# Kernel optimization log

Measured on AMD Instinct MI355X. Metric: run time of the kernel, lower is better.

The kernel has to match this reference:

```python
import jax, jax.numpy as jnp
import numpy as np

B, J, D = 1024, 17, 512          # batch, joints, encoder hidden dim
M, K, DT = 34, 2048, 512         # tokens per pose, codebook size, token dim
DDEC, DDEC_I = 32, 64            # decoder hidden dims
L_ENC, L_DEC = 4, 1
DECAY = 0.9
EPS = 1e-5


def _ln(x, g, b):
    m = jnp.mean(x, -1, keepdims=True)
    v = jnp.mean((x - m) ** 2, -1, keepdims=True)
    return (x - m) * jax.lax.rsqrt(v + EPS) * g + b


def _mlp(x, w1, b1, w2, b2):
    return jax.nn.gelu(x @ w1 + b1, approximate=False) @ w2 + b2


def _mixer(x, p, i):
    ln1g, ln1b, tw1, tb1, tw2, tb2, ln2g, ln2b, cw1, cb1, cw2, cb2 = (a[i] for a in p)
    y = jnp.swapaxes(_ln(x, ln1g, ln1b), 1, 2)        # token-mixing over joints
    y = jnp.swapaxes(_mlp(y, tw1, tb1, tw2, tb2), 1, 2)
    z = _mlp(_ln(x + y, ln2g, ln2b), cw1, cb1, cw2, cb2)  # channel-mixing
    return x + y + z


def _forward(joints, invisible_token, start_w, start_b,
             enc_ln1_g, enc_ln1_b, enc_tw1, enc_tb1, enc_tw2, enc_tb2,
             enc_ln2_g, enc_ln2_b, enc_cw1, enc_cb1, enc_cw2, enc_cb2,
             enc_ln_g, enc_ln_b, token_mlp_w, token_mlp_b, feat_w, feat_b,
             dec_ln1_g, dec_ln1_b, dec_tw1, dec_tb1, dec_tw2, dec_tb2,
             dec_ln2_g, dec_ln2_b, dec_cw1, dec_cb1, dec_cw2, dec_cb2,
             dec_token_mlp_w, dec_token_mlp_b, dec_start_w, dec_start_b,
             dec_ln_g, dec_ln_b, rec_w, rec_b,
             codebook, ema_cluster_size, ema_w):
    x = joints[:, :, :2] @ start_w + start_b                  # [B,J,D]
    vis = (joints[:, :, 2:] != 0).astype(x.dtype)             # [B,J,1]
    x = x * vis + invisible_token * (1.0 - vis)
    encp = (enc_ln1_g, enc_ln1_b, enc_tw1, enc_tb1, enc_tw2, enc_tb2,
            enc_ln2_g, enc_ln2_b, enc_cw1, enc_cb1, enc_cw2, enc_cb2)
    for i in range(L_ENC):
        x = _mixer(x, encp, i)
    x = _ln(x, enc_ln_g, enc_ln_b)
    # token_mlp: Linear over joints axis: [B,D,J] -> [B,D,M] -> [B,M,D]
    x = jnp.einsum('bjd,jm->bmd', x, token_mlp_w) + token_mlp_b[None, :, None]
    feat = (x @ feat_w + feat_b).reshape(B * M, DT)           # encode_feat [N,DT]
    # squared euclidean distances to codebook entries
    dists = (jnp.sum(feat * feat, 1, keepdims=True)
             + jnp.sum(codebook * codebook, 1)
             - 2.0 * feat @ codebook.T)                       # [N,K]
    idx = jnp.argmin(dists, axis=1)                           # [N]
    quant = codebook[idx]                                     # == one_hot(idx) @ codebook
    # EMA codebook update (buffers; single-device so all_reduce == identity)
    sg_feat = jax.lax.stop_gradient(feat)
    counts = jax.ops.segment_sum(jnp.ones((B * M,), feat.dtype), idx, num_segments=K)
    dw = jax.ops.segment_sum(sg_feat, idx, num_segments=K)    # == encodings.T @ feat
    cs = ema_cluster_size * DECAY + (1.0 - DECAY) * counts
    n = jnp.sum(cs)
    cs = (cs + 1e-5) / (n + K * 1e-5) * n                     # laplace smoothing
    ema_w_new = ema_w * DECAY + (1.0 - DECAY) * dw
    codebook_new = ema_w_new / cs[:, None]
    e_latent_loss = jnp.mean(jnp.square(jax.lax.stop_gradient(quant) - feat))
    quant = feat + jax.lax.stop_gradient(quant - feat)        # straight-through
    ptf = quant.reshape(B, M, DT)
    out_ptf = jax.lax.stop_gradient(ptf)
    # decoder_token_mlp: Linear over token axis: [B,DT,M] -> [B,DT,J] -> [B,J,DT]
    y = jnp.einsum('bmd,mj->bjd', ptf, dec_token_mlp_w) + dec_token_mlp_b[None, :, None]
    y = y @ dec_start_w + dec_start_b                         # [B,J,DDEC]
    decp = (dec_ln1_g, dec_ln1_b, dec_tw1, dec_tb1, dec_tw2, dec_tb2,
            dec_ln2_g, dec_ln2_b, dec_cw1, dec_cb1, dec_cw2, dec_cb2)
    for i in range(L_DEC):
        y = _mixer(y, decp, i)
    y = _ln(y, dec_ln_g, dec_ln_b)
    rec = y @ rec_w + rec_b                                   # [B,J,2]
    return rec, idx, e_latent_loss, out_ptf, codebook_new


def setup_inputs():
    ks = iter(jax.random.split(jax.random.key(0), 64))
    def nrm(shape, s=0.02):
        return jax.random.normal(next(ks), shape, jnp.float32) * s
    inp = {}
    coords = jax.random.uniform(next(ks), (B, J, 2), jnp.float32)
    inp['joints'] = jnp.concatenate([coords, jnp.ones((B, J, 1), jnp.float32)], -1)
    inp['joints_feature'] = nrm((B, J, 256), 1.0)   # unused (guide_ratio=0)
    inp['cls_logits'] = jnp.zeros((1, 1), jnp.float32)  # unused in tokenizer stage
    inp['invisible_token'] = nrm((1, 1, D))
    inp['start_w'], inp['start_b'] = nrm((2, D)), jnp.zeros((D,), jnp.float32)
    for pre, L, H, HI in (('enc', L_ENC, D, D), ('dec', L_DEC, DDEC, DDEC_I)):
        inp[pre + '_ln1_g'], inp[pre + '_ln1_b'] = jnp.ones((L, H)), jnp.zeros((L, H))
        inp[pre + '_tw1'], inp[pre + '_tb1'] = nrm((L, J, 64)), jnp.zeros((L, 64))
        inp[pre + '_tw2'], inp[pre + '_tb2'] = nrm((L, 64, J)), jnp.zeros((L, J))
        inp[pre + '_ln2_g'], inp[pre + '_ln2_b'] = jnp.ones((L, H)), jnp.zeros((L, H))
        inp[pre + '_cw1'], inp[pre + '_cb1'] = nrm((L, H, HI)), jnp.zeros((L, HI))
        inp[pre + '_cw2'], inp[pre + '_cb2'] = nrm((L, HI, H)), jnp.zeros((L, H))
    inp['enc_ln_g'], inp['enc_ln_b'] = jnp.ones((D,)), jnp.zeros((D,))
    inp['token_mlp_w'], inp['token_mlp_b'] = nrm((J, M)), jnp.zeros((M,))
    inp['feat_w'], inp['feat_b'] = nrm((D, DT)), jnp.zeros((DT,))
    inp['codebook'] = jax.random.normal(next(ks), (K, DT), jnp.float32)
    inp['ema_cluster_size'] = jnp.zeros((K,), jnp.float32)
    inp['ema_w'] = jax.random.normal(next(ks), (K, DT), jnp.float32)
    inp['dec_token_mlp_w'], inp['dec_token_mlp_b'] = nrm((M, J)), jnp.zeros((J,))
    inp['dec_start_w'], inp['dec_start_b'] = nrm((DT, DDEC)), jnp.zeros((DDEC,))
    inp['dec_ln_g'], inp['dec_ln_b'] = jnp.ones((DDEC,)), jnp.zeros((DDEC,))
    inp['rec_w'], inp['rec_b'] = nrm((DDEC, 2)), jnp.zeros((2,))
    return inp


def reference(joints, joints_feature, cls_logits, invisible_token, start_w, start_b,
              enc_ln1_g, enc_ln1_b, enc_tw1, enc_tb1, enc_tw2, enc_tb2,
              enc_ln2_g, enc_ln2_b, enc_cw1, enc_cb1, enc_cw2, enc_cb2,
              enc_ln_g, enc_ln_b, token_mlp_w, token_mlp_b, feat_w, feat_b,
              codebook, ema_cluster_size, ema_w,
              dec_ln1_g, dec_ln1_b, dec_tw1, dec_tb1, dec_tw2, dec_tb2,
              dec_ln2_g, dec_ln2_b, dec_cw1, dec_cb1, dec_cw2, dec_cb2,
              dec_token_mlp_w, dec_token_mlp_b, dec_start_w, dec_start_b,
              dec_ln_g, dec_ln_b, rec_w, rec_b):
    # joints_feature / cls_logits unused: guide_ratio=0, stage_pct='tokenizer'
    return _forward(joints, invisible_token, start_w, start_b,
                    enc_ln1_g, enc_ln1_b, enc_tw1, enc_tb1, enc_tw2, enc_tb2,
                    enc_ln2_g, enc_ln2_b, enc_cw1, enc_cb1, enc_cw2, enc_cb2,
                    enc_ln_g, enc_ln_b, token_mlp_w, token_mlp_b, feat_w, feat_b,
                    dec_ln1_g, dec_ln1_b, dec_tw1, dec_tb1, dec_tw2, dec_tb2,
                    dec_ln2_g, dec_ln2_b, dec_cw1, dec_cb1, dec_cw2, dec_cb2,
                    dec_token_mlp_w, dec_token_mlp_b, dec_start_w, dec_start_b,
                    dec_ln_g, dec_ln_b, rec_w, rec_b,
                    codebook, ema_cluster_size, ema_w)
```

## Files before the change

### kernel.cpp

```cpp
#include <hip/hip_runtime.h>
#include <math.h>

constexpr int Bn = 1024, Jn = 17, Mn = 34;
constexpr int RJ = Bn * Jn;
constexpr int RM = Bn * Mn;
constexpr size_t SZX = (size_t)RJ * 512;
constexpr size_t SZM = (size_t)RM * 512;

typedef __attribute__((ext_vector_type(8))) short bf16x8;
typedef __attribute__((ext_vector_type(4))) float f32x4;
typedef unsigned long long u64;
typedef unsigned short u16;
typedef unsigned int u32;

__device__ __forceinline__ float gelu_f(float x) {
  return 0.5f * x * (1.0f + erff(x * 0.7071067811865475f));
}
__device__ __forceinline__ u16 bf16_rne(float x) {
  u32 u = __float_as_uint(x);
  u += 0x7fffu + ((u >> 16) & 1u);
  return (u16)(u >> 16);
}
__device__ __forceinline__ float bf16_f(u16 h) {
  return __uint_as_float((u32)h << 16);
}

typedef __attribute__((address_space(1))) const void gas_t;
typedef __attribute__((address_space(3))) void las_t;
__device__ __forceinline__ void gll16(const void* g, void* l) {
  __builtin_amdgcn_global_load_lds((gas_t*)g, (las_t*)l, 16, 0, 0);
}

__global__ __launch_bounds__(256) void embed_kernel(
    const float* __restrict__ joints, const float* __restrict__ inv,
    const float* __restrict__ sw, const float* __restrict__ sb,
    float* __restrict__ out) {
  int tid = blockIdx.x * 256 + threadIdx.x;
  int row = tid >> 9, d = tid & 511;
  float j0 = joints[row * 3 + 0];
  float j1 = joints[row * 3 + 1];
  float j2 = joints[row * 3 + 2];
  float x = fmaf(j0, sw[d], fmaf(j1, sw[512 + d], sb[d]));
  float v = (j2 != 0.0f) ? 1.0f : 0.0f;
  out[tid] = x * v + inv[d] * (1.0f - v);
}

__global__ __launch_bounds__(256) void mixer_fused(
    const float* __restrict__ x_in, float* __restrict__ res_out,
    u16* __restrict__ oh, u16* __restrict__ ol,
    const float* __restrict__ g1, const float* __restrict__ b1,
    const float* __restrict__ tw1, const float* __restrict__ tb1,
    const float* __restrict__ tw2, const float* __restrict__ tb2,
    const float* __restrict__ g2, const float* __restrict__ b2,
    const float* __restrict__ W1, const float* __restrict__ W2,
    u16* __restrict__ Th1, u16* __restrict__ Tl1,
    u16* __restrict__ Th2, u16* __restrict__ Tl2) {
  __shared__ float xs[17][512];
  __shared__ float stats[17][2];
  const int tid = threadIdx.x;
  const int b = blockIdx.x;
  {
    int gid = b * 256 + tid;
    int k = gid >> 9, n = gid & 511;
    float v = W1[gid];
    u16 h = bf16_rne(v);
    Th1[(size_t)n * 512 + k] = h;
    Tl1[(size_t)n * 512 + k] = bf16_rne(v - bf16_f(h));
    v = W2[gid];
    h = bf16_rne(v);
    Th2[(size_t)n * 512 + k] = h;
    Tl2[(size_t)n * 512 + k] = bf16_rne(v - bf16_f(h));
  }
  const float* px = x_in + (size_t)b * 17 * 512;
  for (int i = tid; i < 17 * 512; i += 256) xs[i >> 9][i & 511] = px[i];
  __syncthreads();
  const int wv = tid >> 6, ln_ = tid & 63;
  for (int j = wv; j < 17; j += 4) {
    float v[8];
    float s = 0.0f;
#pragma unroll
    for (int i = 0; i < 8; i++) { v[i] = xs[j][ln_ + 64 * i]; s += v[i]; }
#pragma unroll
    for (int m = 32; m; m >>= 1) s += __shfl_xor(s, m);
    float mean = s * (1.0f / 512.0f);
    float s2 = 0.0f;
#pragma unroll
    for (int i = 0; i < 8; i++) { float t = v[i] - mean; s2 += t * t; }
#pragma unroll
    for (int m = 32; m; m >>= 1) s2 += __shfl_xor(s2, m);
    float rs = 1.0f / sqrtf(s2 * (1.0f / 512.0f) + 1e-5f);
    if (ln_ == 0) { stats[j][0] = mean; stats[j][1] = rs; }
  }
  __syncthreads();
  {
    const int d0 = tid, d1 = tid + 256;
    float ga = g1[d0], ba = b1[d0];
    float gb = g1[d1], bb2 = b1[d1];
    float t0[17], t1[17], a0[17], a1[17];
#pragma unroll
    for (int j = 0; j < 17; j++) {
      float mj = stats[j][0], rj = stats[j][1];
      t0[j] = (xs[j][d0] - mj) * rj * ga + ba;
      t1[j] = (xs[j][d1] - mj) * rj * gb + bb2;
      a0[j] = 0.0f; a1[j] = 0.0f;
    }
#pragma unroll 1
    for (int k = 0; k < 64; k++) {
      float h0 = tb1[k], h1 = h0;
#pragma unroll
      for (int j = 0; j < 17; j++) {
        float w = tw1[j * 64 + k];
        h0 = fmaf(t0[j], w, h0);
        h1 = fmaf(t1[j], w, h1);
      }
      h0 = gelu_f(h0);
      h1 = gelu_f(h1);
#pragma unroll
      for (int j = 0; j < 17; j++) {
        float w = tw2[k * 17 + j];
        a0[j] = fmaf(h0, w, a0[j]);
        a1[j] = fmaf(h1, w, a1[j]);
      }
    }
#pragma unroll
    for (int j = 0; j < 17; j++) {
      float tb = tb2[j];
      float r0 = xs[j][d0] + a0[j] + tb;
      float r1 = xs[j][d1] + a1[j] + tb;
      xs[j][d0] = r0;
      xs[j][d1] = r1;
      res_out[((size_t)b * 17 + j) * 512 + d0] = r0;
      res_out[((size_t)b * 17 + j) * 512 + d1] = r1;
    }
  }
  __syncthreads();
  for (int j = wv; j < 17; j += 4) {
    float v[8];
    float s = 0.0f;
#pragma unroll
    for (int i = 0; i < 8; i++) { v[i] = xs[j][ln_ + 64 * i]; s += v[i]; }
#pragma unroll
    for (int m = 32; m; m >>= 1) s += __shfl_xor(s, m);
    float mean = s * (1.0f / 512.0f);
    float s2 = 0.0f;
#pragma unroll
    for (int i = 0; i < 8; i++) { float t = v[i] - mean; s2 += t * t; }
#pragma unroll
    for (int m = 32; m; m >>= 1) s2 += __shfl_xor(s2, m);
    float rs = 1.0f / sqrtf(s2 * (1.0f / 512.0f) + 1e-5f);
#pragma unroll
    for (int i = 0; i < 8; i++) {
      int d = ln_ + 64 * i;
      float o = (v[i] - mean) * rs * g2[d] + b2[d];
      u16 h = bf16_rne(o);
      size_t off = ((size_t)b * 17 + j) * 512 + d;
      oh[off] = h;
      ol[off] = bf16_rne(o - bf16_f(h));
    }
  }
}

__global__ __launch_bounds__(256) void lnmix_fused(
    const float* __restrict__ x_in, u16* __restrict__ oh, u16* __restrict__ ol,
    const float* __restrict__ g, const float* __restrict__ bb,
    const float* __restrict__ w, const float* __restrict__ bias,
    const float* __restrict__ Wf, u16* __restrict__ Thf, u16* __restrict__ Tlf) {
  __shared__ float xs[17][513];
  const int tid = threadIdx.x;
  const int b = blockIdx.x;
  {
    int gid = b * 256 + tid;
    int k = gid >> 9, n = gid & 511;
    float v = Wf[gid];
    u16 h = bf16_rne(v);
    Thf[(size_t)n * 512 + k] = h;
    Tlf[(size_t)n * 512 + k] = bf16_rne(v - bf16_f(h));
  }
  const float* px = x_in + (size_t)b * 17 * 512;
  for (int i = tid; i < 17 * 512; i += 256) xs[i >> 9][i & 511] = px[i];
  __syncthreads();
  const int wv = tid >> 6, ln_ = tid & 63;
  for (int j = wv; j < 17; j += 4) {
    float v[8];
    float s = 0.0f;
#pragma unroll
    for (int i = 0; i < 8; i++) { v[i] = xs[j][ln_ + 64 * i]; s += v[i]; }
#pragma unroll
    for (int m = 32; m; m >>= 1) s += __shfl_xor(s, m);
    float mean = s * (1.0f / 512.0f);
    float s2 = 0.0f;
#pragma unroll
    for (int i = 0; i < 8; i++) { float t = v[i] - mean; s2 += t * t; }
#pragma unroll
    for (int m = 32; m; m >>= 1) s2 += __shfl_xor(s2, m);
    float rs = 1.0f / sqrtf(s2 * (1.0f / 512.0f) + 1e-5f);
#pragma unroll
    for (int i = 0; i < 8; i++) {
      int d = ln_ + 64 * i;
      xs[j][d] = (v[i] - mean) * rs * g[d] + bb[d];
    }
  }
  __syncthreads();
  {
    const int d0 = tid, d1 = tid + 256;
    float t0[17], t1[17];
#pragma unroll
    for (int j = 0; j < 17; j++) { t0[j] = xs[j][d0]; t1[j] = xs[j][d1]; }
#pragma unroll 1
    for (int m = 0; m < 34; m++) {
      float s0 = bias[m], s1 = s0;
#pragma unroll
      for (int j = 0; j < 17; j++) {
        float wv2 = w[j * 34 + m];
        s0 = fmaf(t0[j], wv2, s0);
        s1 = fmaf(t1[j], wv2, s1);
      }
      size_t o0 = ((size_t)b * 34 + m) * 512 + d0;
      u16 h0 = bf16_rne(s0);
      oh[o0] = h0;
      ol[o0] = bf16_rne(s0 - bf16_f(h0));
      size_t o1 = o0 + 256;
      u16 h1 = bf16_rne(s1);
      oh[o1] = h1;
      ol[o1] = bf16_rne(s1 - bf16_f(h1));
    }
  }
}

__global__ __launch_bounds__(256) void splitnorm_kernel(
    const float* __restrict__ CBm, u16* __restrict__ hi, u16* __restrict__ lo,
    float* __restrict__ cnorm, u64* __restrict__ packed, int* __restrict__ cnt) {
  int gid = blockIdx.x * 256 + threadIdx.x;
  for (int i = gid; i < RM; i += 131072) packed[i] = ~0ull;
  if (gid < 2048) cnt[gid] = 0;
  int wave = threadIdx.x >> 6, lane = threadIdx.x & 63;
  int k = blockIdx.x * 4 + wave;
  const float4* p4 = (const float4*)(CBm + (size_t)k * 512);
  ushort4* h4 = (ushort4*)(hi + (size_t)k * 512);
  ushort4* l4 = (ushort4*)(lo + (size_t)k * 512);
  float s = 0.0f;
#pragma unroll
  for (int i = 0; i < 2; i++) {
    float4 x = p4[lane + 64 * i];
    ushort4 h, l;
    h.x = bf16_rne(x.x); l.x = bf16_rne(x.x - bf16_f(h.x));
    h.y = bf16_rne(x.y); l.y = bf16_rne(x.y - bf16_f(h.y));
    h.z = bf16_rne(x.z); l.z = bf16_rne(x.z - bf16_f(h.z));
    h.w = bf16_rne(x.w); l.w = bf16_rne(x.w - bf16_f(h.w));
    h4[lane + 64 * i] = h;
    l4[lane + 64 * i] = l;
    s = fmaf(x.x, x.x, s); s = fmaf(x.y, x.y, s);
    s = fmaf(x.z, x.z, s); s = fmaf(x.w, x.w, s);
  }
#pragma unroll
  for (int m = 32; m; m >>= 1) s += __shfl_xor(s, m);
  if (lane == 0) cnorm[k] = s;
}

template <int GELU_FLAG, int RES_FLAG, int HILO_OUT>
__global__ __launch_bounds__(256, 4) void mgemm64(
    const u16* __restrict__ Ah, const u16* __restrict__ Al,
    const u16* __restrict__ Bh, const u16* __restrict__ Bl,
    const float* __restrict__ bias, const float* __restrict__ R,
    float* __restrict__ C, u16* __restrict__ Oh, u16* __restrict__ Ol, int N) {
  __shared__ __align__(16) u16 sAh[2048], sAl[2048], sBh[4096], sBl[4096];
  const int tid = threadIdx.x;
  const int m0 = blockIdx.x * 64, n0 = blockIdx.y * 128;
  const int lane = tid & 63, wave = tid >> 6;
  const int wm = wave >> 1, wn = wave & 1;
  const int fr = lane & 15, q = lane >> 4;
  const int ra = tid >> 2, ca = (tid & 3) ^ ((ra >> 1) & 3);
  const size_t aoff = (size_t)(m0 + ra) * 512 + ca * 8;
  const int rb0 = tid >> 2, cb0 = (tid & 3) ^ ((rb0 >> 1) & 3);
  const int ci1 = tid + 256;
  const int rb1 = ci1 >> 2, cb1 = (ci1 & 3) ^ ((rb1 >> 1) & 3);
  const size_t boff0 = (size_t)(n0 + rb0) * 512 + cb0 * 8;
  const size_t boff1 = (size_t)(n0 + rb1) * 512 + cb1 * 8;
  const int ldA = wave * 512;
  const int ldB0 = wave * 512, ldB1 = 2048 + wave * 512;
  int fca[2], fcb[4];
#pragma unroll
  for (int mt = 0; mt < 2; mt++) {
    int rra = wm * 32 + mt * 16 + fr;
    fca[mt] = (rra * 4 + (q ^ ((rra >> 1) & 3))) * 8;
  }
#pragma unroll
  for (int nt = 0; nt < 4; nt++) {
    int rrb = wn * 64 + nt * 16 + fr;
    fcb[nt] = (rrb * 4 + (q ^ ((rrb >> 1) & 3))) * 8;
  }
  f32x4 acc[2][4];
#pragma unroll
  for (int i = 0; i < 2; i++)
#pragma unroll
    for (int j = 0; j < 4; j++) {
      acc[i][j][0] = 0.0f; acc[i][j][1] = 0.0f;
      acc[i][j][2] = 0.0f; acc[i][j][3] = 0.0f;
    }
  for (int k0 = 0; k0 < 512; k0 += 32) {
    gll16(Ah + aoff + k0, &sAh[ldA]);
    gll16(Al + aoff + k0, &sAl[ldA]);
    gll16(Bh + boff0 + k0, &sBh[ldB0]);
    gll16(Bh + boff1 + k0, &sBh[ldB1]);
    gll16(Bl + boff0 + k0, &sBl[ldB0]);
    gll16(Bl + boff1 + k0, &sBl[ldB1]);
    __syncthreads();
    bf16x8 fah[2], fal[2], fbh[4], fbl[4];
#pragma unroll
    for (int mt = 0; mt < 2; mt++) {
      fah[mt] = *(const bf16x8*)&sAh[fca[mt]];
      fal[mt] = *(const bf16x8*)&sAl[fca[mt]];
    }
#pragma unroll
    for (int nt = 0; nt < 4; nt++) {
      fbh[nt] = *(const bf16x8*)&sBh[fcb[nt]];
      fbl[nt] = *(const bf16x8*)&sBl[fcb[nt]];
    }
#pragma unroll
    for (int mt = 0; mt < 2; mt++)
#pragma unroll
      for (int nt = 0; nt < 4; nt++) {
        acc[mt][nt] = __builtin_amdgcn_mfma_f32_16x16x32_bf16(
            fah[mt], fbh[nt], acc[mt][nt], 0, 0, 0);
        acc[mt][nt] = __builtin_amdgcn_mfma_f32_16x16x32_bf16(
            fah[mt], fbl[nt], acc[mt][nt], 0, 0, 0);
        acc[mt][nt] = __builtin_amdgcn_mfma_f32_16x16x32_bf16(
            fal[mt], fbh[nt], acc[mt][nt], 0, 0, 0);
      }
    __syncthreads();
  }
#pragma unroll
  for (int mt = 0; mt < 2; mt++)
#pragma unroll
    for (int reg = 0; reg < 4; reg++) {
      int row = m0 + wm * 32 + mt * 16 + q * 4 + reg;
#pragma unroll
      for (int nt = 0; nt < 4; nt++) {
        int col = n0 + wn * 64 + nt * 16 + fr;
        float v = acc[mt][nt][reg] + bias[col];
        if (GELU_FLAG) v = gelu_f(v);
        if (RES_FLAG) v += R[(size_t)row * N + col];
        if (HILO_OUT) {
          u16 h = bf16_rne(v);
          Oh[(size_t)row * N + col] = h;
          Ol[(size_t)row * N + col] = bf16_rne(v - bf16_f(h));
        } else {
          C[(size_t)row * N + col] = v;
        }
      }
    }
}

#define MG_PROLOGUE()                                                        \
  const int tid = threadIdx.x;                                               \
  const int m0 = blockIdx.x * 128, n0 = blockIdx.y * 128;                    \
  const int lane = tid & 63, wave = tid >> 6;                                \
  const int wm = wave >> 1, wn = wave & 1;                                   \
  const int fr = lane & 15, q = lane >> 4, qd = q;                           \
  const int ci0 = wave * 128 + lane, ci1 = ci0 + 64;                         \
  const int r0 = ci0 >> 2, c0x = (ci0 & 3) ^ ((r0 >> 1) & 3);                \
  const int r1 = ci1 >> 2, c1x = (ci1 & 3) ^ ((r1 >> 1) & 3);                \
  const size_t aoff0 = (size_t)(m0 + r0) * 512 + c0x * 8;                    \
  const size_t aoff1 = (size_t)(m0 + r1) * 512 + c1x * 8;                    \
  const size_t boff0 = (size_t)(n0 + r0) * 512 + c0x * 8;                    \
  const size_t boff1 = (size_t)(n0 + r1) * 512 + c1x * 8;                    \
  const int ld0 = wave * 1024, ld1 = ld0 + 512;       \
  int fca[4], fcb[4];                                                        \
  _Pragma("unroll") for (int t4 = 0; t4 < 4; t4++) {                         \
    int rra = wm * 64 + t4 * 16 + fr;                                        \
    int rrb = wn * 64 + t4 * 16 + fr;                                        \
    int sz = q ^ ((fr >> 1) & 3);                                            \
    fca[t4] = (rra * 4 + sz) * 8;                                            \
    fcb[t4] = (rrb * 4 + sz) * 8;                                            \
  }                                                                          \
  f32x4 acc[4][4];                                                           \
  _Pragma("unroll") for (int i = 0; i < 4; i++)                              \
    _Pragma("unroll") for (int j = 0; j < 4; j++) {                          \
      acc[i][j][0] = 0.0f; acc[i][j][1] = 0.0f;                              \
      acc[i][j][2] = 0.0f; acc[i][j][3] = 0.0f;                              \
    }

#define MG_KLOOP(Ah, Al, Bh, Bl)                                             \
  for (int k0 = 0; k0 < 512; k0 += 32) {                                     \
    gll16(Ah + aoff0 + k0, &sAh[ld0]);                                       \
    gll16(Ah + aoff1 + k0, &sAh[ld1]);                                       \
    gll16(Al + aoff0 + k0, &sAl[ld0]);                                       \
    gll16(Al + aoff1 + k0, &sAl[ld1]);                                       \
    gll16(Bh + boff0 + k0, &sBh[ld0]);                                       \
    gll16(Bh + boff1 + k0, &sBh[ld1]);                                       \
    gll16(Bl + boff0 + k0, &sBl[ld0]);                                       \
    gll16(Bl + boff1 + k0, &sBl[ld1]);                                       \
    __syncthreads();                                                         \
    bf16x8 fah[4], fal[4], fbh[4], fbl[4];                                   \
    _Pragma("unroll") for (int t4 = 0; t4 < 4; t4++) {                       \
      fah[t4] = *(const bf16x8*)&sAh[fca[t4]];                               \
      fal[t4] = *(const bf16x8*)&sAl[fca[t4]];                               \
      fbh[t4] = *(const bf16x8*)&sBh[fcb[t4]];                               \
      fbl[t4] = *(const bf16x8*)&sBl[fcb[t4]];                               \
    }                                                                        \
    _Pragma("unroll") for (int mt = 0; mt < 4; mt++)                         \
      _Pragma("unroll") for (int nt = 0; nt < 4; nt++) {                     \
        acc[mt][nt] = __builtin_amdgcn_mfma_f32_16x16x32_bf16(               \
            fah[mt], fbh[nt], acc[mt][nt], 0, 0, 0);                         \
        acc[mt][nt] = __builtin_amdgcn_mfma_f32_16x16x32_bf16(               \
            fah[mt], fbl[nt], acc[mt][nt], 0, 0, 0);                         \
        acc[mt][nt] = __builtin_amdgcn_mfma_f32_16x16x32_bf16(               \
            fal[mt], fbh[nt], acc[mt][nt], 0, 0, 0);                         \
      }                                                                      \
    __syncthreads();                                                         \
  }

__global__ __launch_bounds__(256, 4) void dist_mfma(
    const u16* __restrict__ Ah, const u16* __restrict__ Al,
    const u16* __restrict__ Bh, const u16* __restrict__ Bl,
    const float* __restrict__ cnorm, u64* __restrict__ packed) {
  __shared__ __align__(16) u16 sAh[4096], sAl[4096], sBh[4096], sBl[4096];
  MG_PROLOGUE()
  MG_KLOOP(Ah, Al, Bh, Bl)
#pragma unroll
  for (int mt = 0; mt < 4; mt++)
#pragma unroll
    for (int reg = 0; reg < 4; reg++) {
      u64 best = ~0ull;
#pragma unroll
      for (int nt = 0; nt < 4; nt++) {
        int c = n0 + wn * 64 + nt * 16 + fr;
        float d = cnorm[c] - 2.0f * acc[mt][nt][reg];
        u32 ub = __float_as_uint(d);
        ub = (ub & 0x80000000u) ? ~ub : (ub | 0x80000000u);
        u64 p = ((u64)ub << 32) | (u32)c;
        best = (p < best) ? p : best;
      }
#pragma unroll
      for (int mm = 1; mm <= 8; mm <<= 1) {
        u32 h2 = __shfl_xor((u32)(best >> 32), mm);
        u32 l2 = __shfl_xor((u32)best, mm);
        u64 o = ((u64)h2 << 32) | l2;
        best = (o < best) ? o : best;
      }
      if (fr == 0) {
        int row = m0 + wm * 64 + mt * 16 + qd * 4 + reg;
        atomicMin(&packed[row], best);
      }
    }
}

__global__ __launch_bounds__(256) void idxcount_kernel(
    const u64* __restrict__ packed, float* __restrict__ o_idx,
    int* __restrict__ cnt) {
  __shared__ int h[2048];
  for (int i = threadIdx.x; i < 2048; i += 256) h[i] = 0;
  __syncthreads();
  int r = blockIdx.x * 256 + threadIdx.x;
  u32 k = (u32)packed[r];
  o_idx[r] = (float)k;
  atomicAdd(&h[k], 1);
  __syncthreads();
  for (int i = threadIdx.x; i < 2048; i += 256) {
    int v = h[i];
    if (v) atomicAdd(&cnt[i], v);
  }
}

__global__ __launch_bounds__(256) void scan_kernel(
    const int* __restrict__ cnt, int* __restrict__ base,
    int* __restrict__ cursor, const float* __restrict__ ema_cs,
    float* __restrict__ nbuf) {
  __shared__ int part[256];
  __shared__ float esum[256];
  int t = threadIdx.x;
  int local[8];
  int s = 0;
  float es = 0.0f;
#pragma unroll
  for (int i = 0; i < 8; i++) {
    local[i] = cnt[t * 8 + i];
    s += local[i];
    es += ema_cs[t * 8 + i];
  }
  part[t] = s;
  esum[t] = es;
  __syncthreads();
  for (int off = 1; off < 256; off <<= 1) {
    int v = (t >= off) ? part[t - off] : 0;
    __syncthreads();
    part[t] += v;
    __syncthreads();
  }
  int run = part[t] - s;
#pragma unroll
  for (int i = 0; i < 8; i++) {
    base[t * 8 + i] = run;
    cursor[t * 8 + i] = run;
    run += local[i];
  }
  for (int o = 128; o; o >>= 1) {
    if (t < o) esum[t] += esum[t + o];
    __syncthreads();
  }
  if (t == 0) nbuf[0] = 0.9f * esum[0] + 0.1f * (float)RM;
}

__global__ __launch_bounds__(256) void scatter_kernel(
    const u64* __restrict__ packed, int* __restrict__ cursor,
    u32* __restrict__ bucket, float* __restrict__ dw) {
  __shared__ int h[2048];
  __shared__ int gb[2048];
  int gid = blockIdx.x * 256 + threadIdx.x;
  for (int i = gid; i < 2048 * 512; i += RM) dw[i] = 0.0f;
  for (int i = threadIdx.x; i < 2048; i += 256) h[i] = 0;
  __syncthreads();
  int k = (int)(u32)packed[gid];
  int lrank = atomicAdd(&h[k], 1);
  __syncthreads();
  for (int i = threadIdx.x; i < 2048; i += 256) {
    int v = h[i];
    gb[i] = v ? atomicAdd(&cursor[i], v) : 0;
  }
  __syncthreads();
  bucket[gb[k] + lrank] = ((u32)k << 17) | (u32)gid;
}

__global__ __launch_bounds__(256) void quant_out_kernel(
    const u16* __restrict__ fh, const u16* __restrict__ fl,
    const float* __restrict__ CBm, const u64* __restrict__ packed,
    float* __restrict__ ptf_out, float* __restrict__ lpart) {
  __shared__ float wred[4];
  int row = blockIdx.x * 2 + (threadIdx.x >> 7);
  int t = threadIdx.x & 127;
  int k = (int)(u32)packed[row];
  uint2 hb = ((const uint2*)(fh + (size_t)row * 512))[t];
  uint2 lb = ((const uint2*)(fl + (size_t)row * 512))[t];
  float f0 = bf16_f((u16)hb.x) + bf16_f((u16)lb.x);
  float f1 = bf16_f((u16)(hb.x >> 16)) + bf16_f((u16)(lb.x >> 16));
  float f2 = bf16_f((u16)hb.y) + bf16_f((u16)lb.y);
  float f3 = bf16_f((u16)(hb.y >> 16)) + bf16_f((u16)(lb.y >> 16));
  float4 c = ((const float4*)(CBm + (size_t)k * 512))[t];
  float* po = ptf_out + (size_t)row * 512 + 4 * t;
  po[0] = c.x; po[1] = c.y; po[2] = c.z; po[3] = c.w;
  float dx = c.x - f0, dy = c.y - f1, dz = c.z - f2, dwv = c.w - f3;
  float ls = dx * dx + dy * dy + dz * dz + dwv * dwv;
#pragma unroll
  for (int m = 32; m; m >>= 1) ls += __shfl_xor(ls, m);
  if ((threadIdx.x & 63) == 0) wred[threadIdx.x >> 6] = ls;
  __syncthreads();
  if (threadIdx.x == 0)
    lpart[blockIdx.x] = wred[0] + wred[1] + wred[2] + wred[3];
}

__global__ __launch_bounds__(256) void dwsum_chunk_kernel(
    const u16* __restrict__ fh, const u16* __restrict__ fl,
    const u32* __restrict__ bucket, float* __restrict__ dw) {
  __shared__ u32 sp[64];
  const int t = threadIdx.x;
  if (t < 64) sp[t] = bucket[blockIdx.x * 64 + t];
  __syncthreads();
  float ax = 0.0f, ay = 0.0f;
  int curk = (int)(sp[0] >> 17);
  u32 hb = *(const u32*)(fh + (size_t)(sp[0] & 0x1FFFF) * 512 + 2 * t);
  u32 lb = *(const u32*)(fl + (size_t)(sp[0] & 0x1FFFF) * 512 + 2 * t);
  for (int i = 0; i < 64; i++) {
    u32 hn = 0, ln2 = 0;
    if (i + 1 < 64) {
      hn = *(const u32*)(fh + (size_t)(sp[i + 1] & 0x1FFFF) * 512 + 2 * t);
      ln2 = *(const u32*)(fl + (size_t)(sp[i + 1] & 0x1FFFF) * 512 + 2 * t);
    }
    int k = (int)(sp[i] >> 17);
    if (k != curk) {
      atomicAdd(&dw[(size_t)curk * 512 + 2 * t], ax);
      atomicAdd(&dw[(size_t)curk * 512 + 2 * t + 1], ay);
      ax = 0.0f; ay = 0.0f; curk = k;
    }
    ax += bf16_f((u16)hb) + bf16_f((u16)lb);
    ay += bf16_f((u16)(hb >> 16)) + bf16_f((u16)(lb >> 16));
    hb = hn; lb = ln2;
  }
  atomicAdd(&dw[(size_t)curk * 512 + 2 * t], ax);
  atomicAdd(&dw[(size_t)curk * 512 + 2 * t + 1], ay);
}

__global__ __launch_bounds__(256) void cbnew_kernel(
    const float* __restrict__ ema_w, const float* __restrict__ dw,
    const float* __restrict__ ema_cs, const int* __restrict__ cnt,
    const float* __restrict__ nbuf, float* __restrict__ outp,
    const float* __restrict__ lpart, float* __restrict__ loss_out) {
  int tid = blockIdx.x * 256 + threadIdx.x;
  int k = tid >> 9;
  float n = nbuf[0];
  float cs = ema_cs[k] * 0.9f + 0.1f * (float)cnt[k];
  cs = (cs + 1e-5f) / (n + 0.02048f) * n;
  outp[tid] = (ema_w[tid] * 0.9f + 0.1f * dw[tid]) / cs;
  if (blockIdx.x == 0) {
    __shared__ float red[256];
    float s = 0.0f;
    for (int i = threadIdx.x; i < RM / 2; i += 256) s += lpart[i];
    red[threadIdx.x] = s;
    __syncthreads();
    for (int o = 128; o; o >>= 1) {
      if (threadIdx.x < o) red[threadIdx.x] += red[threadIdx.x + o];
      __syncthreads();
    }
    if (threadIdx.x == 0)
      loss_out[0] = red[0] / (float)((size_t)RM * 512);
  }
}

__global__ __launch_bounds__(256) void decoder_fused(
    const float* __restrict__ ptf,
    const float* __restrict__ dtokw, const float* __restrict__ dtokb,
    const float* __restrict__ dsw, const float* __restrict__ dsb,
    const float* __restrict__ ln1g, const float* __restrict__ ln1b,
    const float* __restrict__ tw1, const float* __restrict__ tb1,
    const float* __restrict__ tw2, const float* __restrict__ tb2,
    const float* __restrict__ ln2g, const float* __restrict__ ln2b,
    const float* __restrict__ cw1, const float* __restrict__ cb1,
    const float* __restrict__ cw2, const float* __restrict__ cb2,
    const float* __restrict__ lng, const float* __restrict__ lnb,
    const float* __restrict__ recw, const float* __restrict__ recb,
    float* __restrict__ o_rec) {
  __shared__ float yS[17][260];
  __shared__ float zS[17][33];
  __shared__ float t2S[17][33];
  __shared__ float hS[17][65];
  const int tid = threadIdx.x;
  const int b = blockIdx.x;
  float zacc0 = 0.0f, zacc1 = 0.0f, zacc2 = 0.0f;
  const int j0 = tid >> 5, dd0 = tid & 31;
  const int j1 = (tid + 256) >> 5;
  const int j2 = (tid + 512) >> 5;
  for (int ch = 0; ch < 2; ch++) {
    float p[34];
#pragma unroll
    for (int m = 0; m < 34; m++)
      p[m] = ptf[((size_t)b * 34 + m) * 512 + ch * 256 + tid];
#pragma unroll 1
    for (int j = 0; j < 17; j++) {
      float s = dtokb[j];
#pragma unroll
      for (int m = 0; m < 34; m++) s = fmaf(p[m], dtokw[m * 17 + j], s);
      yS[j][tid] = s;
    }
    __syncthreads();
    {
      const float4* y0 = (const float4*)&yS[j0][0];
      const float4* y1 = (const float4*)&yS[j1][0];
      const float* wg = dsw + (size_t)ch * 256 * 32 + dd0;
#pragma unroll 1
      for (int d4 = 0; d4 < 64; d4++) {
        float4 va = y0[d4];
        float4 vb = y1[d4];
        float w0 = wg[(4 * d4 + 0) * 32];
        float w1 = wg[(4 * d4 + 1) * 32];
        float w2 = wg[(4 * d4 + 2) * 32];
        float w3 = wg[(4 * d4 + 3) * 32];
        zacc0 = fmaf(va.x, w0, zacc0); zacc0 = fmaf(va.y, w1, zacc0);
        zacc0 = fmaf(va.z, w2, zacc0); zacc0 = fmaf(va.w, w3, zacc0);
        zacc1 = fmaf(vb.x, w0, zacc1); zacc1 = fmaf(vb.y, w1, zacc1);
        zacc1 = fmaf(vb.z, w2, zacc1); zacc1 = fmaf(vb.w, w3, zacc1);
      }
      if (tid < 32) {
        const float4* y2 = (const float4*)&yS[j2][0];
#pragma unroll 1
        for (int d4 = 0; d4 < 64; d4++) {
          float4 vc = y2[d4];
          float w0 = wg[(4 * d4 + 0) * 32];
          float w1 = wg[(4 * d4 + 1) * 32];
          float w2 = wg[(4 * d4 + 2) * 32];
          float w3 = wg[(4 * d4 + 3) * 32];
          zacc2 = fmaf(vc.x, w0, zacc2); zacc2 = fmaf(vc.y, w1, zacc2);
          zacc2 = fmaf(vc.z, w2, zacc2); zacc2 = fmaf(vc.w, w3, zacc2);
        }
      }
    }
    __syncthreads();
  }
  zS[j0][dd0] = zacc0 + dsb[dd0];
  zS[j1][dd0] = zacc1 + dsb[dd0];
  if (tid < 32) zS[j2][dd0] = zacc2 + dsb[dd0];
  __syncthreads();
  if (tid < 17) {
    float m = 0.0f;
#pragma unroll
    for (int d = 0; d < 32; d++) m += zS[tid][d];
    m *= (1.0f / 32.0f);
    float v = 0.0f;
#pragma unroll
    for (int d = 0; d < 32; d++) { float t = zS[tid][d] - m; v += t * t; }
    float rs = 1.0f / sqrtf(v * (1.0f / 32.0f) + 1e-5f);
#pragma unroll
    for (int d = 0; d < 32; d++)
      t2S[tid][d] = (zS[tid][d] - m) * rs * ln1g[d] + ln1b[d];
  }
  __syncthreads();
  if (tid < 32) {
    float t[17], acc[17];
#pragma unroll
    for (int j = 0; j < 17; j++) { t[j] = t2S[j][tid]; acc[j] = 0.0f; }
    for (int k = 0; k < 64; k++) {
      float h = tb1[k];
#pragma unroll
      for (int j = 0; j < 17; j++) h = fmaf(t[j], tw1[j * 64 + k], h);
      h = gelu_f(h);
#pragma unroll
      for (int j = 0; j < 17; j++) acc[j] = fmaf(h, tw2[k * 17 + j], acc[j]);
    }
#pragma unroll
    for (int j = 0; j < 17; j++) zS[j][tid] = zS[j][tid] + acc[j] + tb2[j];
  }
  __syncthreads();
  if (tid < 17) {
    float m = 0.0f;
#pragma unroll
    for (int d = 0; d < 32; d++) m += zS[tid][d];
    m *= (1.0f / 32.0f);
    float v = 0.0f;
#pragma unroll
    for (int d = 0; d < 32; d++) { float t = zS[tid][d] - m; v += t * t; }
    float rs = 1.0f / sqrtf(v * (1.0f / 32.0f) + 1e-5f);
#pragma unroll
    for (int d = 0; d < 32; d++)
      t2S[tid][d] = (zS[tid][d] - m) * rs * ln2g[d] + ln2b[d];
  }
  __syncthreads();
  for (int p = tid; p < 17 * 64; p += 256) {
    int j = p >> 6, k = p & 63;
    float s = cb1[k];
#pragma unroll
    for (int d = 0; d < 32; d++) s = fmaf(t2S[j][d], cw1[d * 64 + k], s);
    hS[j][k] = gelu_f(s);
  }
  __syncthreads();
  {
    float cb = cb2[dd0];
    float s0 = cb, s1 = cb;
#pragma unroll
    for (int k = 0; k < 64; k++) {
      float w = cw2[k * 32 + dd0];
      s0 = fmaf(hS[j0][k], w, s0);
      s1 = fmaf(hS[j1][k], w, s1);
    }
    zS[j0][dd0] += s0;
    zS[j1][dd0] += s1;
    if (tid < 32) {
      float s2 = cb;
#pragma unroll
      for (int k = 0; k < 64; k++) s2 = fmaf(hS[j2][k], cw2[k * 32 + dd0], s2);
      zS[j2][dd0] += s2;
    }
  }
  __syncthreads();
  if (tid < 17) {
    float m = 0.0f;
#pragma unroll
    for (int d = 0; d < 32; d++) m += zS[tid][d];
    m *= (1.0f / 32.0f);
    float v = 0.0f;
#pragma unroll
    for (int d = 0; d < 32; d++) { float t = zS[tid][d] - m; v += t * t; }
    float rs = 1.0f / sqrtf(v * (1.0f / 32.0f) + 1e-5f);
#pragma unroll
    for (int d = 0; d < 32; d++)
      t2S[tid][d] = (zS[tid][d] - m) * rs * lng[d] + lnb[d];
  }
  __syncthreads();
  if (tid < 34) {
    int j = tid >> 1, c = tid & 1;
    float s = recb[c];
#pragma unroll
    for (int d = 0; d < 32; d++) s = fmaf(t2S[j][d], recw[d * 2 + c], s);
    o_rec[((size_t)b * 17 + j) * 2 + c] = s;
  }
}

extern "C" void kernel_launch(void* const* d_in, const int* in_sizes, int n_in,
                              void* d_out, int out_size, void* d_ws, size_t ws_size,
                              hipStream_t stream) {
  const float* joints   = (const float*)d_in[0];
  const float* inv_tok  = (const float*)d_in[3];
  const float* start_w  = (const float*)d_in[4];
  const float* start_b  = (const float*)d_in[5];
  const float* e_ln1g = (const float*)d_in[6];
  const float* e_ln1b = (const float*)d_in[7];
  const float* e_tw1  = (const float*)d_in[8];
  const float* e_tb1  = (const float*)d_in[9];
  const float* e_tw2  = (const float*)d_in[10];
  const float* e_tb2  = (const float*)d_in[11];
  const float* e_ln2g = (const float*)d_in[12];
  const float* e_ln2b = (const float*)d_in[13];
  const float* e_cw1  = (const float*)d_in[14];
  const float* e_cb1  = (const float*)d_in[15];
  const float* e_cw2  = (const float*)d_in[16];
  const float* e_cb2  = (const float*)d_in[17];
  const float* d_ln1g = (const float*)d_in[18];
  const float* d_ln1b = (const float*)d_in[19];
  const float* d_tw1  = (const float*)d_in[20];
  const float* d_tb1  = (const float*)d_in[21];
  const float* d_tw2  = (const float*)d_in[22];
  const float* d_tb2  = (const float*)d_in[23];
  const float* d_ln2g = (const float*)d_in[24];
  const float* d_ln2b = (const float*)d_in[25];
  const float* d_cw1  = (const float*)d_in[26];
  const float* d_cb1  = (const float*)d_in[27];
  const float* d_cw2  = (const float*)d_in[28];
  const float* d_cb2  = (const float*)d_in[29];
  const float* enc_lng = (const float*)d_in[30];
  const float* enc_lnb = (const float*)d_in[31];
  const float* tok_w   = (const float*)d_in[32];
  const float* tok_b   = (const float*)d_in[33];
  const float* feat_w  = (const float*)d_in[34];
  const float* feat_b  = (const float*)d_in[35];
  const float* codebook = (const float*)d_in[36];
  const float* ema_cs   = (const float*)d_in[37];
  const float* ema_w    = (const float*)d_in[38];
  const float* dtok_w   = (const float*)d_in[39];
  const float* dtok_b   = (const float*)d_in[40];
  const float* dstart_w = (const float*)d_in[41];
  const float* dstart_b = (const float*)d_in[42];
  const float* dec_lng  = (const float*)d_in[43];
  const float* dec_lnb  = (const float*)d_in[44];
  const float* rec_w    = (const float*)d_in[45];
  const float* rec_b    = (const float*)d_in[46];

  float* ws = (float*)d_ws;
  float* Ab  = ws;
  float* Bb  = ws + SZX;
  float* Cc  = ws + 2 * SZX;
  float* P1e = ws + 3 * SZX;
  float* P2e = ws + 4 * SZX;
  float* cbs = ws + 5 * SZX;
  float* cnorm = cbs + 1048576;
  u64*  packed = (u64*)(cnorm + 2048);
  int*  cnt    = (int*)(cnorm + 2048 + 69632);
  int*  basebuf = cnt + 2048;
  int*  cursor  = basebuf + 2048;
  u32*  bucket  = (u32*)(cursor + 2048);
  float* lpart  = (float*)(bucket + RM);
  float* nbuf   = lpart + RM / 2;
  float* dw     = nbuf + 2048;
  u16* WTh1 = (u16*)dw;
  u16* WTl1 = (u16*)(dw + 131072);
  u16* WTh2 = (u16*)(dw + 262144);
  u16* WTl2 = (u16*)(dw + 393216);
  u16* P1eh = (u16*)P1e;  u16* P1el = (u16*)(P1e + SZX / 2);
  u16* P2eh = (u16*)P2e;  u16* P2el = (u16*)(P2e + SZX / 2);
  u16* P1mh = (u16*)Ab;   u16* P1ml = (u16*)Bb;
  u16* P2mh = (u16*)Cc;   u16* P2ml = (u16*)P1e;
  u16* chh = (u16*)cbs;   u16* cll = (u16*)(cbs + 524288);

  float* outp = (float*)d_out;
  float* o_rec = outp;
  float* o_idx = outp + (size_t)RJ * 2;
  float* o_loss = o_idx + RM;
  float* o_ptf = o_loss + 1;
  float* o_cb = o_ptf + SZM;

  embed_kernel<<<(RJ * 512) / 256, 256, 0, stream>>>(joints, inv_tok, start_w, start_b, Ab);
  for (int i = 0; i < 4; i++) {
    mixer_fused<<<Bn, 256, 0, stream>>>(
        Ab, Bb, P1eh, P1el,
        e_ln1g + i * 512, e_ln1b + i * 512,
        e_tw1 + i * 17 * 64, e_tb1 + i * 64, e_tw2 + i * 64 * 17, e_tb2 + i * 17,
        e_ln2g + i * 512, e_ln2b + i * 512,
        e_cw1 + (size_t)i * 512 * 512, e_cw2 + (size_t)i * 512 * 512,
        WTh1, WTl1, WTh2, WTl2);
    mgemm64<1, 0, 1><<<dim3(RJ / 64, 4), 256, 0, stream>>>(
        P1eh, P1el, WTh1, WTl1, e_cb1 + i * 512, nullptr, nullptr, P2eh, P2el, 512);
    mgemm64<0, 1, 0><<<dim3(RJ / 64, 4), 256, 0, stream>>>(
        P2eh, P2el, WTh2, WTl2, e_cb2 + i * 512, Bb, Ab, nullptr, nullptr, 512);
  }
  lnmix_fused<<<Bn, 256, 0, stream>>>(Ab, P1mh, P1ml, enc_lng, enc_lnb, tok_w, tok_b,
                                      feat_w, WTh1, WTl1);
  mgemm64<0, 0, 1><<<dim3(RM / 64, 4), 256, 0, stream>>>(
      P1mh, P1ml, WTh1, WTl1, feat_b, nullptr, nullptr, P2mh, P2ml, 512);

  splitnorm_kernel<<<2048 / 4, 256, 0, stream>>>(codebook, chh, cll, cnorm, packed, cnt);
  dist_mfma<<<dim3(RM / 128, 2048 / 128), 256, 0, stream>>>(P2mh, P2ml, chh, cll, cnorm, packed);

  idxcount_kernel<<<RM / 256, 256, 0, stream>>>(packed, o_idx, cnt);
  scan_kernel<<<1, 256, 0, stream>>>(cnt, basebuf, cursor, ema_cs, nbuf);
  scatter_kernel<<<RM / 256, 256, 0, stream>>>(packed, cursor, bucket, dw);
  quant_out_kernel<<<RM / 2, 256, 0, stream>>>(P2mh, P2ml, codebook, packed, o_ptf, lpart);
  dwsum_chunk_kernel<<<RM / 64, 256, 0, stream>>>(P2mh, P2ml, bucket, dw);
  cbnew_kernel<<<(2048 * 512) / 256, 256, 0, stream>>>(
      ema_w, dw, ema_cs, cnt, nbuf, o_cb, lpart, o_loss);

  decoder_fused<<<Bn, 256, 0, stream>>>(
      o_ptf, dtok_w, dtok_b, dstart_w, dstart_b,
      d_ln1g, d_ln1b, d_tw1, d_tb1, d_tw2, d_tb2, d_ln2g, d_ln2b,
      d_cw1, d_cb1, d_cw2, d_cb2, dec_lng, dec_lnb, rec_w, rec_b, o_rec);
}
```

Baseline: 1.361 ms.

## Fuse embed into first mixer, merge quant output into dwsum, split dist launch

The embedding is now computed directly into shared memory inside the first mixer launch, which removes a separate kernel and a round trip of the activation tensor through global memory. Quantized-output writing and the commitment-loss partial sums move into the bucketed dwsum kernel, so the quant_out kernel and its second read of the features disappear. The codebook-distance kernel is split into two launches over codebook halves, with the occupancy hint raised from 4 to 5 blocks. The split launch relies on atomic-min style packing into the same buffer across both launches, and the loss reduction bound changes to match the new number of partials.

```diff
diff --git a/kernel.cpp b/kernel.cpp
--- a/kernel.cpp
+++ b/kernel.cpp
@@ -31,20 +31,7 @@
   __builtin_amdgcn_global_load_lds((gas_t*)g, (las_t*)l, 16, 0, 0);
 }
 
-__global__ __launch_bounds__(256) void embed_kernel(
-    const float* __restrict__ joints, const float* __restrict__ inv,
-    const float* __restrict__ sw, const float* __restrict__ sb,
-    float* __restrict__ out) {
-  int tid = blockIdx.x * 256 + threadIdx.x;
-  int row = tid >> 9, d = tid & 511;
-  float j0 = joints[row * 3 + 0];
-  float j1 = joints[row * 3 + 1];
-  float j2 = joints[row * 3 + 2];
-  float x = fmaf(j0, sw[d], fmaf(j1, sw[512 + d], sb[d]));
-  float v = (j2 != 0.0f) ? 1.0f : 0.0f;
-  out[tid] = x * v + inv[d] * (1.0f - v);
-}
-
+template <int EMBED>
 __global__ __launch_bounds__(256) void mixer_fused(
     const float* __restrict__ x_in, float* __restrict__ res_out,
     u16* __restrict__ oh, u16* __restrict__ ol,
@@ -54,7 +41,9 @@
     const float* __restrict__ g2, const float* __restrict__ b2,
     const float* __restrict__ W1, const float* __restrict__ W2,
     u16* __restrict__ Th1, u16* __restrict__ Tl1,
-    u16* __restrict__ Th2, u16* __restrict__ Tl2) {
+    u16* __restrict__ Th2, u16* __restrict__ Tl2,
+    const float* __restrict__ joints, const float* __restrict__ inv_tok,
+    const float* __restrict__ swg, const float* __restrict__ sbg) {
   __shared__ float xs[17][512];
   __shared__ float stats[17][2];
   const int tid = threadIdx.x;
@@ -71,8 +60,18 @@
     Th2[(size_t)n * 512 + k] = h;
     Tl2[(size_t)n * 512 + k] = bf16_rne(v - bf16_f(h));
   }
-  const float* px = x_in + (size_t)b * 17 * 512;
-  for (int i = tid; i < 17 * 512; i += 256) xs[i >> 9][i & 511] = px[i];
+  if (EMBED) {
+    for (int i = tid; i < 17 * 512; i += 256) {
+      int j = i >> 9, d = i & 511;
+      const float* jp = joints + ((size_t)b * 17 + j) * 3;
+      float x = fmaf(jp[0], swg[d], fmaf(jp[1], swg[512 + d], sbg[d]));
+      float vis = (jp[2] != 0.0f) ? 1.0f : 0.0f;
+      xs[j][d] = x * vis + inv_tok[d] * (1.0f - vis);
+    }
+  } else {
+    const float* px = x_in + (size_t)b * 17 * 512;
+    for (int i = tid; i < 17 * 512; i += 256) xs[i >> 9][i & 511] = px[i];
+  }
   __syncthreads();
   const int wv = tid >> 6, ln_ = tid & 63;
   for (int j = wv; j < 17; j += 4) {
@@ -353,7 +352,7 @@
 
 #define MG_PROLOGUE()                                                        \
   const int tid = threadIdx.x;                                               \
-  const int m0 = blockIdx.x * 128, n0 = blockIdx.y * 128;                    \
+  const int m0 = blockIdx.x * 128, n0 = (blockIdx.y + n_base) * 128;         \
   const int lane = tid & 63, wave = tid >> 6;                                \
   const int wm = wave >> 1, wn = wave & 1;                                   \
   const int fr = lane & 15, q = lane >> 4, qd = q;                           \
@@ -410,10 +409,10 @@
     __syncthreads();                                                         \
   }
 
-__global__ __launch_bounds__(256, 4) void dist_mfma(
+__global__ __launch_bounds__(256, 5) void dist_mfma(
     const u16* __restrict__ Ah, const u16* __restrict__ Al,
     const u16* __restrict__ Bh, const u16* __restrict__ Bl,
-    const float* __restrict__ cnorm, u64* __restrict__ packed) {
+    const float* __restrict__ cnorm, u64* __restrict__ packed, int n_base) {
   __shared__ __align__(16) u16 sAh[4096], sAl[4096], sBh[4096], sBl[4096];
   MG_PROLOGUE()
   MG_KLOOP(Ah, Al, Bh, Bl)
@@ -521,42 +520,20 @@
   bucket[gb[k] + lrank] = ((u32)k << 17) | (u32)gid;
 }
 
-__global__ __launch_bounds__(256) void quant_out_kernel(
-    const u16* __restrict__ fh, const u16* __restrict__ fl,
-    const float* __restrict__ CBm, const u64* __restrict__ packed,
-    float* __restrict__ ptf_out, float* __restrict__ lpart) {
-  __shared__ float wred[4];
-  int row = blockIdx.x * 2 + (threadIdx.x >> 7);
-  int t = threadIdx.x & 127;
-  int k = (int)(u32)packed[row];
-  uint2 hb = ((const uint2*)(fh + (size_t)row * 512))[t];
-  uint2 lb = ((const uint2*)(fl + (size_t)row * 512))[t];
-  float f0 = bf16_f((u16)hb.x) + bf16_f((u16)lb.x);
-  float f1 = bf16_f((u16)(hb.x >> 16)) + bf16_f((u16)(lb.x >> 16));
-  float f2 = bf16_f((u16)hb.y) + bf16_f((u16)lb.y);
-  float f3 = bf16_f((u16)(hb.y >> 16)) + bf16_f((u16)(lb.y >> 16));
-  float4 c = ((const float4*)(CBm + (size_t)k * 512))[t];
-  float* po = ptf_out + (size_t)row * 512 + 4 * t;
-  po[0] = c.x; po[1] = c.y; po[2] = c.z; po[3] = c.w;
-  float dx = c.x - f0, dy = c.y - f1, dz = c.z - f2, dwv = c.w - f3;
-  float ls = dx * dx + dy * dy + dz * dz + dwv * dwv;
-#pragma unroll
-  for (int m = 32; m; m >>= 1) ls += __shfl_xor(ls, m);
-  if ((threadIdx.x & 63) == 0) wred[threadIdx.x >> 6] = ls;
-  __syncthreads();
-  if (threadIdx.x == 0)
-    lpart[blockIdx.x] = wred[0] + wred[1] + wred[2] + wred[3];
-}
-
 __global__ __launch_bounds__(256) void dwsum_chunk_kernel(
     const u16* __restrict__ fh, const u16* __restrict__ fl,
-    const u32* __restrict__ bucket, float* __restrict__ dw) {
+    const u32* __restrict__ bucket, const float* __restrict__ CBm,
+    float* __restrict__ dw, float* __restrict__ ptf_out,
+    float* __restrict__ lpart) {
   __shared__ u32 sp[64];
+  __shared__ float wred[4];
   const int t = threadIdx.x;
   if (t < 64) sp[t] = bucket[blockIdx.x * 64 + t];
   __syncthreads();
-  float ax = 0.0f, ay = 0.0f;
+  float ax = 0.0f, ay = 0.0f, lacc = 0.0f;
   int curk = (int)(sp[0] >> 17);
+  float c0 = CBm[(size_t)curk * 512 + 2 * t];
+  float c1 = CBm[(size_t)curk * 512 + 2 * t + 1];
   u32 hb = *(const u32*)(fh + (size_t)(sp[0] & 0x1FFFF) * 512 + 2 * t);
   u32 lb = *(const u32*)(fl + (size_t)(sp[0] & 0x1FFFF) * 512 + 2 * t);
   for (int i = 0; i < 64; i++) {
@@ -570,13 +547,27 @@
       atomicAdd(&dw[(size_t)curk * 512 + 2 * t], ax);
       atomicAdd(&dw[(size_t)curk * 512 + 2 * t + 1], ay);
       ax = 0.0f; ay = 0.0f; curk = k;
-    }
-    ax += bf16_f((u16)hb) + bf16_f((u16)lb);
-    ay += bf16_f((u16)(hb >> 16)) + bf16_f((u16)(lb >> 16));
+      c0 = CBm[(size_t)k * 512 + 2 * t];
+      c1 = CBm[(size_t)k * 512 + 2 * t + 1];
+    }
+    float f0 = bf16_f((u16)hb) + bf16_f((u16)lb);
+    float f1 = bf16_f((u16)(hb >> 16)) + bf16_f((u16)(lb >> 16));
+    ax += f0;
+    ay += f1;
+    int row = (int)(sp[i] & 0x1FFFF);
+    ptf_out[(size_t)row * 512 + 2 * t] = c0;
+    ptf_out[(size_t)row * 512 + 2 * t + 1] = c1;
+    float e0 = c0 - f0, e1 = c1 - f1;
+    lacc = fmaf(e0, e0, fmaf(e1, e1, lacc));
     hb = hn; lb = ln2;
   }
   atomicAdd(&dw[(size_t)curk * 512 + 2 * t], ax);
   atomicAdd(&dw[(size_t)curk * 512 + 2 * t + 1], ay);
+#pragma unroll
+  for (int m = 32; m; m >>= 1) lacc += __shfl_xor(lacc, m);
+  if ((t & 63) == 0) wred[t >> 6] = lacc;
+  __syncthreads();
+  if (t == 0) lpart[blockIdx.x] = wred[0] + wred[1] + wred[2] + wred[3];
 }
 
 __global__ __launch_bounds__(256) void cbnew_kernel(
@@ -593,7 +584,7 @@
   if (blockIdx.x == 0) {
     __shared__ float red[256];
     float s = 0.0f;
-    for (int i = threadIdx.x; i < RM / 2; i += 256) s += lpart[i];
+    for (int i = threadIdx.x; i < RM / 64; i += 256) s += lpart[i];
     red[threadIdx.x] = s;
     __syncthreads();
     for (int o = 128; o; o >>= 1) {
@@ -854,15 +845,22 @@
   float* o_ptf = o_loss + 1;
   float* o_cb = o_ptf + SZM;
 
-  embed_kernel<<<(RJ * 512) / 256, 256, 0, stream>>>(joints, inv_tok, start_w, start_b, Ab);
   for (int i = 0; i < 4; i++) {
-    mixer_fused<<<Bn, 256, 0, stream>>>(
-        Ab, Bb, P1eh, P1el,
-        e_ln1g + i * 512, e_ln1b + i * 512,
-        e_tw1 + i * 17 * 64, e_tb1 + i * 64, e_tw2 + i * 64 * 17, e_tb2 + i * 17,
-        e_ln2g + i * 512, e_ln2b + i * 512,
-        e_cw1 + (size_t)i * 512 * 512, e_cw2 + (size_t)i * 512 * 512,
-        WTh1, WTl1, WTh2, WTl2);
+    if (i == 0) {
+      mixer_fused<1><<<Bn, 256, 0, stream>>>(
+          nullptr, Bb, P1eh, P1el,
+          e_ln1g, e_ln1b, e_tw1, e_tb1, e_tw2, e_tb2, e_ln2g, e_ln2b,
+          e_cw1, e_cw2, WTh1, WTl1, WTh2, WTl2,
+          joints, inv_tok, start_w, start_b);
+    } else {
+      mixer_fused<0><<<Bn, 256, 0, stream>>>(
+          Ab, Bb, P1eh, P1el,
+          e_ln1g + i * 512, e_ln1b + i * 512,
+          e_tw1 + i * 17 * 64, e_tb1 + i * 64, e_tw2 + i * 64 * 17, e_tb2 + i * 17,
+          e_ln2g + i * 512, e_ln2b + i * 512,
+          e_cw1 + (size_t)i * 512 * 512, e_cw2 + (size_t)i * 512 * 512,
+          WTh1, WTl1, WTh2, WTl2, nullptr, nullptr, nullptr, nullptr);
+    }
     mgemm64<1, 0, 1><<<dim3(RJ / 64, 4), 256, 0, stream>>>(
         P1eh, P1el, WTh1, WTl1, e_cb1 + i * 512, nullptr, nullptr, P2eh, P2el, 512);
     mgemm64<0, 1, 0><<<dim3(RJ / 64, 4), 256, 0, stream>>>(
@@ -874,13 +872,14 @@
       P1mh, P1ml, WTh1, WTl1, feat_b, nullptr, nullptr, P2mh, P2ml, 512);
 
   splitnorm_kernel<<<2048 / 4, 256, 0, stream>>>(codebook, chh, cll, cnorm, packed, cnt);
-  dist_mfma<<<dim3(RM / 128, 2048 / 128), 256, 0, stream>>>(P2mh, P2ml, chh, cll, cnorm, packed);
+  dist_mfma<<<dim3(RM / 128, 8), 256, 0, stream>>>(P2mh, P2ml, chh, cll, cnorm, packed, 0);
+  dist_mfma<<<dim3(RM / 128, 8), 256, 0, stream>>>(P2mh, P2ml, chh, cll, cnorm, packed, 8);
 
   idxcount_kernel<<<RM / 256, 256, 0, stream>>>(packed, o_idx, cnt);
   scan_kernel<<<1, 256, 0, stream>>>(cnt, basebuf, cursor, ema_cs, nbuf);
   scatter_kernel<<<RM / 256, 256, 0, stream>>>(packed, cursor, bucket, dw);
-  quant_out_kernel<<<RM / 2, 256, 0, stream>>>(P2mh, P2ml, codebook, packed, o_ptf, lpart);
-  dwsum_chunk_kernel<<<RM / 64, 256, 0, stream>>>(P2mh, P2ml, bucket, dw);
+  dwsum_chunk_kernel<<<RM / 64, 256, 0, stream>>>(
+      P2mh, P2ml, bucket, codebook, dw, o_ptf, lpart);
   cbnew_kernel<<<(2048 * 512) / 256, 256, 0, stream>>>(
       ema_w, dw, ema_cs, cnt, nbuf, o_cb, lpart, o_loss);
 
```

Result: slower. 2.411 ms (+77.2%).
